# Kernel tuning notes

Measured on AMD Instinct MI355X. Metric: run time of the kernel, lower is better.

Reference implementation:

```python
import jax, jax.numpy as jnp
import numpy as np

BN_EPS = 1e-5
NEG_SLOPE = 0.2

def _avgpool2(x):
    B, C, H, W = x.shape
    return x.reshape(B, C, H // 2, 2, W // 2, 2).mean(axis=(3, 5))

def _conv1x1(x, w, b):
    # x: [B,C,H,W], w: [O,C], b: [O]
    return jnp.einsum('bchw,oc->bohw', x, w) + b[None, :, None, None]

def _bilinear_resize(x, out_h, out_w):
    # PyTorch F.interpolate(mode='bilinear', align_corners=False) semantics
    B, C, h, w = x.shape
    ys = jnp.maximum((jnp.arange(out_h, dtype=jnp.float32) + 0.5) * (h / out_h) - 0.5, 0.0)
    xs = jnp.maximum((jnp.arange(out_w, dtype=jnp.float32) + 0.5) * (w / out_w) - 0.5, 0.0)
    y0 = jnp.floor(ys).astype(jnp.int32); x0 = jnp.floor(xs).astype(jnp.int32)
    wy = (ys - y0.astype(jnp.float32)).astype(x.dtype)
    wx = (xs - x0.astype(jnp.float32)).astype(x.dtype)
    y1 = jnp.minimum(y0 + 1, h - 1); x1 = jnp.minimum(x0 + 1, w - 1)
    rows = x[:, :, y0, :] * (1.0 - wy)[None, None, :, None] + x[:, :, y1, :] * wy[None, None, :, None]
    out = rows[:, :, :, x0] * (1.0 - wx)[None, None, None, :] + rows[:, :, :, x1] * wx[None, None, None, :]
    return out

def setup_inputs() -> dict:
    key = jax.random.key(0)
    ks = jax.random.split(key, 16)
    B, Cin, Hid, Cout, H, W = 8, 64, 64, 64, 128, 128
    s = 0.05
    return {
        'rgb': jax.random.normal(ks[0], (B, Cin, H, W), dtype=jnp.float32),
        'freq': jax.random.normal(ks[1], (B, Cin, H, W), dtype=jnp.float32),
        'w_q': jax.random.normal(ks[2], (Hid, Cin), dtype=jnp.float32) * s,
        'b_q': jax.random.normal(ks[3], (Hid,), dtype=jnp.float32) * s,
        'w_k': jax.random.normal(ks[4], (Hid, Cin), dtype=jnp.float32) * s,
        'b_k': jax.random.normal(ks[5], (Hid,), dtype=jnp.float32) * s,
        'w_v': jax.random.normal(ks[6], (Hid, Cin), dtype=jnp.float32) * s,
        'b_v': jax.random.normal(ks[7], (Hid,), dtype=jnp.float32) * s,
        'w_o': jax.random.normal(ks[8], (Cout, Hid), dtype=jnp.float32) * s,
        'b_o': jax.random.normal(ks[9], (Cout,), dtype=jnp.float32) * s,
        'bn_gamma': jnp.ones((Cout,), dtype=jnp.float32),
        'bn_beta': jnp.zeros((Cout,), dtype=jnp.float32),
        'bn_mean': jax.random.normal(ks[10], (Cout,), dtype=jnp.float32) * s,
        'bn_var': jax.random.uniform(ks[11], (Cout,), dtype=jnp.float32, minval=0.5, maxval=1.5),
    }

def reference(rgb, freq, w_q, b_q, w_k, b_k, w_v, b_v, w_o, b_o, bn_gamma, bn_beta, bn_mean, bn_var):
    B, C, H, W = rgb.shape
    rgb_ds = _avgpool2(rgb)
    freq_ds = _avgpool2(freq)
    hd, wd = rgb_ds.shape[2], rgb_ds.shape[3]
    hid = w_q.shape[0]
    scale = hid ** (-0.5)
    # 1x1 conv QKV projections, flatten spatial dims to tokens N = hd*wd
    q = _conv1x1(rgb_ds, w_q, b_q).reshape(B, hid, hd * wd)   # [B,hid,N]
    k = _conv1x1(freq_ds, w_k, b_k).reshape(B, hid, hd * wd)  # [B,hid,N]
    v = _conv1x1(freq_ds, w_v, b_v).reshape(B, hid, hd * wd)  # [B,hid,N]
    attn = jax.nn.softmax(jnp.einsum('bcn,bcm->bnm', q, k) * scale, axis=-1)  # [B,N,N]
    z = jnp.einsum('bnm,bcm->bcn', attn, v).reshape(B, hid, hd, wd)
    z = _bilinear_resize(z, H, W)
    y = _conv1x1(z, w_o, b_o)
    # inference-mode BatchNorm fused as affine
    inv = bn_gamma / jnp.sqrt(bn_var + BN_EPS)
    y = (y - bn_mean[None, :, None, None]) * inv[None, :, None, None] + bn_beta[None, :, None, None]
    y = jnp.where(y >= 0, y, NEG_SLOPE * y)  # LeakyReLU(0.2)
    return rgb + y
```

## Files before the change

kernel.cpp:

```cpp
#include <hip/hip_runtime.h>
#include <hip/hip_bf16.h>

typedef unsigned short u16;
typedef unsigned int   u32;
typedef __attribute__((ext_vector_type(8))) short bf16x8;
typedef __attribute__((ext_vector_type(4))) float f32x4;

__device__ __forceinline__ u16 f2bf(float f) {
  u32 u = __float_as_uint(f);
  u32 r = u + 0x7fffu + ((u >> 16) & 1u);
  return (u16)(r >> 16);
}
__device__ __forceinline__ float bflo(u32 u) { return __uint_as_float(u << 16); }
__device__ __forceinline__ float bfhi(u32 u) { return __uint_as_float(u & 0xffff0000u); }
__device__ __forceinline__ u32 packhi(float a, float b) {
  return __builtin_amdgcn_perm(__float_as_uint(b), __float_as_uint(a), 0x07060302u);
}

__global__ __launch_bounds__(256, 4) void k_qkv(
    const float* __restrict__ rgb, const float* __restrict__ freq,
    const float* __restrict__ wq, const float* __restrict__ bq,
    const float* __restrict__ wk, const float* __restrict__ bk,
    const float* __restrict__ wv, const float* __restrict__ bv,
    u16* __restrict__ Qo, u16* __restrict__ Ko, u16* __restrict__ Vo)
{
  __shared__ __align__(16) u16 sm[3 * 4608];
  u16* X  = sm;
  u16* W0 = sm + 4608;
  u16* W1 = sm + 9216;

  const int t    = threadIdx.x;
  const int side = blockIdx.x & 1;
  const int seg  = blockIdx.x >> 1;
  const int idx0 = seg * 64;
  const int bb   = idx0 >> 12;
  const int n0   = idx0 & 4095;
  const int h    = n0 >> 6;
  const float* src = side ? freq : rgb;

  const size_t sbase = (size_t)bb * 64 * 16384 + (size_t)(2 * h) * 128;
  for (int i = 0; i < 2; ++i) {
    int cell = i * 256 + t;
    int tok  = cell & 63;
    int grp  = cell >> 6;
    const float* p0 = src + sbase + 2 * tok + (size_t)(grp * 8) * 16384;
    u32 pk[4];
#pragma unroll
    for (int cc = 0; cc < 8; cc += 2) {
      const float* pa = p0 + (size_t)cc * 16384;
      float2 a0 = *(const float2*)pa;
      float2 a1 = *(const float2*)(pa + 128);
      float v0 = 0.25f * ((a0.x + a0.y) + (a1.x + a1.y));
      const float* pb = pa + 16384;
      float2 b0 = *(const float2*)pb;
      float2 b1 = *(const float2*)(pb + 128);
      float v1 = 0.25f * ((b0.x + b0.y) + (b1.x + b1.y));
      pk[cc >> 1] = (u32)f2bf(v0) | ((u32)f2bf(v1) << 16);
    }
    uint4 q4; q4.x = pk[0]; q4.y = pk[1]; q4.z = pk[2]; q4.w = pk[3];
    *(uint4*)&X[tok * 72 + grp * 8] = q4;
  }
  {
    const int o = t >> 2, c0 = (t & 3) << 4;
    const float4* p4 = (const float4*)((side ? wk : wq) + o * 64 + c0);
    float4 f0 = p4[0], f1 = p4[1], f2 = p4[2], f3 = p4[3];
    uint4 qa, qb;
    qa.x = (u32)f2bf(f0.x) | ((u32)f2bf(f0.y) << 16);
    qa.y = (u32)f2bf(f0.z) | ((u32)f2bf(f0.w) << 16);
    qa.z = (u32)f2bf(f1.x) | ((u32)f2bf(f1.y) << 16);
    qa.w = (u32)f2bf(f1.z) | ((u32)f2bf(f1.w) << 16);
    qb.x = (u32)f2bf(f2.x) | ((u32)f2bf(f2.y) << 16);
    qb.y = (u32)f2bf(f2.z) | ((u32)f2bf(f2.w) << 16);
    qb.z = (u32)f2bf(f3.x) | ((u32)f2bf(f3.y) << 16);
    qb.w = (u32)f2bf(f3.z) | ((u32)f2bf(f3.w) << 16);
    *(uint4*)&W0[o * 72 + c0] = qa;
    *(uint4*)&W0[o * 72 + c0 + 8] = qb;
    if (side) {
      const float4* v4 = (const float4*)(wv + o * 64 + c0);
      float4 g0 = v4[0], g1 = v4[1], g2 = v4[2], g3 = v4[3];
      qa.x = (u32)f2bf(g0.x) | ((u32)f2bf(g0.y) << 16);
      qa.y = (u32)f2bf(g0.z) | ((u32)f2bf(g0.w) << 16);
      qa.z = (u32)f2bf(g1.x) | ((u32)f2bf(g1.y) << 16);
      qa.w = (u32)f2bf(g1.z) | ((u32)f2bf(g1.w) << 16);
      qb.x = (u32)f2bf(g2.x) | ((u32)f2bf(g2.y) << 16);
      qb.y = (u32)f2bf(g2.z) | ((u32)f2bf(g2.w) << 16);
      qb.z = (u32)f2bf(g3.x) | ((u32)f2bf(g3.y) << 16);
      qb.w = (u32)f2bf(g3.z) | ((u32)f2bf(g3.w) << 16);
      *(uint4*)&W1[o * 72 + c0] = qa;
      *(uint4*)&W1[o * 72 + c0 + 8] = qb;
    }
  }
  __syncthreads();

  const int lane = t & 63, w = t >> 6;
  const int l15 = lane & 15, qd = lane >> 4;
  const int tb = w * 16;

  bf16x8 af0 = *(const bf16x8*)&X[(tb + l15) * 72 + qd * 8];
  bf16x8 af1 = *(const bf16x8*)&X[(tb + l15) * 72 + 32 + qd * 8];

  f32x4 acc[4];
#pragma unroll
  for (int nt = 0; nt < 4; ++nt) {
    bf16x8 b0 = *(const bf16x8*)&W0[(nt * 16 + l15) * 72 + qd * 8];
    bf16x8 b1 = *(const bf16x8*)&W0[(nt * 16 + l15) * 72 + 32 + qd * 8];
    f32x4 a = {0.f, 0.f, 0.f, 0.f};
    a = __builtin_amdgcn_mfma_f32_16x16x32_bf16(af0, b0, a, 0, 0, 0);
    a = __builtin_amdgcn_mfma_f32_16x16x32_bf16(af1, b1, a, 0, 0, 0);
    acc[nt] = a;
  }
  {
    const float* bias0 = side ? bk : bq;
    const float sc = side ? 1.f : 0.125f;
    u16* dst0 = side ? Ko : Qo;
#pragma unroll
    for (int nt = 0; nt < 4; ++nt) {
      float bia = bias0[nt * 16 + l15];
#pragma unroll
      for (int e = 0; e < 4; ++e) {
        int tok = idx0 + tb + qd * 4 + e;
        dst0[(size_t)tok * 64 + nt * 16 + l15] = f2bf((acc[nt][e] + bia) * sc);
      }
    }
  }

  if (side) {
    f32x4 accv[4];
#pragma unroll
    for (int ct = 0; ct < 4; ++ct) {
      bf16x8 a0 = *(const bf16x8*)&W1[(ct * 16 + l15) * 72 + qd * 8];
      bf16x8 a1 = *(const bf16x8*)&W1[(ct * 16 + l15) * 72 + 32 + qd * 8];
      f32x4 a = {0.f, 0.f, 0.f, 0.f};
      a = __builtin_amdgcn_mfma_f32_16x16x32_bf16(a0, af0, a, 0, 0, 0);
      a = __builtin_amdgcn_mfma_f32_16x16x32_bf16(a1, af1, a, 0, 0, 0);
      accv[ct] = a;
    }
#pragma unroll
    for (int ct = 0; ct < 4; ++ct) {
#pragma unroll
      for (int e = 0; e < 4; ++e) {
        int c = ct * 16 + qd * 4 + e;
        float v = accv[ct][e] + bv[c];
        Vo[((size_t)(bb * 64 + c)) * 4096 + n0 + tb + l15] = f2bf(v);
      }
    }
  }
}

__global__ __launch_bounds__(256, 2) void k_attn(
    const u16* __restrict__ Qg, const u16* __restrict__ Kg,
    const u16* __restrict__ Vg,
    const float* __restrict__ wo, const float* __restrict__ bo,
    const float* __restrict__ gam, const float* __restrict__ bet,
    const float* __restrict__ mean, const float* __restrict__ var,
    u16* __restrict__ Ya)
{
  __shared__ __align__(16) u16 Pb[4 * 4608];
  __shared__ __align__(16) u16 Wl[4608];
  __shared__ __align__(16) u16 Zc[4608];
  __shared__ float lb[256];

  const int b  = blockIdx.x;
  const int q0 = blockIdx.y * 64;
  const int t  = threadIdx.x;
  const int lane = t & 63, w = t >> 6;
  const int l15 = lane & 15, qd = lane >> 4;
  u16* P = Pb + w * 4608;

  {
    const int o = t >> 2, c0 = (t & 3) << 4;
    const float4* p4 = (const float4*)(wo + o * 64 + c0);
    float4 f0 = p4[0], f1 = p4[1], f2 = p4[2], f3 = p4[3];
    uint4 qa, qb;
    qa.x = (u32)f2bf(f0.x) | ((u32)f2bf(f0.y) << 16);
    qa.y = (u32)f2bf(f0.z) | ((u32)f2bf(f0.w) << 16);
    qa.z = (u32)f2bf(f1.x) | ((u32)f2bf(f1.y) << 16);
    qa.w = (u32)f2bf(f1.z) | ((u32)f2bf(f1.w) << 16);
    qb.x = (u32)f2bf(f2.x) | ((u32)f2bf(f2.y) << 16);
    qb.y = (u32)f2bf(f2.z) | ((u32)f2bf(f2.w) << 16);
    qb.z = (u32)f2bf(f3.x) | ((u32)f2bf(f3.y) << 16);
    qb.w = (u32)f2bf(f3.z) | ((u32)f2bf(f3.w) << 16);
    *(uint4*)&Wl[o * 72 + c0] = qa;
    *(uint4*)&Wl[o * 72 + c0 + 8] = qb;
  }

  bf16x8 qf[4][2];
#pragma unroll
  for (int qt = 0; qt < 4; ++qt) {
    const u16* p = Qg + ((size_t)(b * 4096 + q0 + qt * 16 + l15)) * 64 + qd * 8;
    qf[qt][0] = *(const bf16x8*)p;
    qf[qt][1] = *(const bf16x8*)(p + 32);
  }

  f32x4 zacc[4][4];
#pragma unroll
  for (int i = 0; i < 4; ++i)
#pragma unroll
    for (int j = 0; j < 4; ++j) {
      f32x4 z = {0.f, 0.f, 0.f, 0.f};
      zacc[i][j] = z;
    }
  float lacc[4] = {0.f, 0.f, 0.f, 0.f};

  for (int tile = 0; tile < 16; ++tile) {
    const int n0 = w * 1024 + tile * 64;

    bf16x8 kf[4][2], vf[4][2];
#pragma unroll
    for (int mt = 0; mt < 4; ++mt) {
      const u16* p = Kg + ((size_t)(b * 4096 + n0 + mt * 16 + l15)) * 64 + qd * 8;
      kf[mt][0] = *(const bf16x8*)p;
      kf[mt][1] = *(const bf16x8*)(p + 32);
    }
#pragma unroll
    for (int ct = 0; ct < 4; ++ct) {
      const u16* p = Vg + ((size_t)(b * 64 + ct * 16 + l15)) * 4096 + n0 + qd * 8;
      vf[ct][0] = *(const bf16x8*)p;
      vf[ct][1] = *(const bf16x8*)(p + 32);
    }

#pragma unroll
    for (int qt = 0; qt < 4; ++qt) {
#pragma unroll
      for (int mt = 0; mt < 4; ++mt) {
        f32x4 a = {0.f, 0.f, 0.f, 0.f};
        a = __builtin_amdgcn_mfma_f32_16x16x32_bf16(kf[mt][0], qf[qt][0], a, 0, 0, 0);
        a = __builtin_amdgcn_mfma_f32_16x16x32_bf16(kf[mt][1], qf[qt][1], a, 0, 0, 0);
        float p0 = __expf(a[0]);
        float p1 = __expf(a[1]);
        float p2 = __expf(a[2]);
        float p3 = __expf(a[3]);
        lacc[qt] += (p0 + p1) + (p2 + p3);
        uint2 pw;
        pw.x = packhi(p0, p1);
        pw.y = packhi(p2, p3);
        *(uint2*)&P[(qt * 16 + l15) * 72 + mt * 16 + qd * 4] = pw;
      }
    }
#pragma unroll
    for (int qt = 0; qt < 4; ++qt) {
      bf16x8 pf0 = *(const bf16x8*)&P[(qt * 16 + l15) * 72 + qd * 8];
      bf16x8 pf1 = *(const bf16x8*)&P[(qt * 16 + l15) * 72 + 32 + qd * 8];
#pragma unroll
      for (int ct = 0; ct < 4; ++ct) {
        zacc[ct][qt] = __builtin_amdgcn_mfma_f32_16x16x32_bf16(vf[ct][0], pf0, zacc[ct][qt], 0, 0, 0);
        zacc[ct][qt] = __builtin_amdgcn_mfma_f32_16x16x32_bf16(vf[ct][1], pf1, zacc[ct][qt], 0, 0, 0);
      }
    }
  }

#pragma unroll
  for (int qt = 0; qt < 4; ++qt) {
    float l = lacc[qt];
    l += __shfl_xor(l, 16);
    l += __shfl_xor(l, 32);
    lb[w * 64 + qt * 16 + l15] = l;
  }
#pragma unroll
  for (int qt = 0; qt < 4; ++qt)
#pragma unroll
    for (int ct = 0; ct < 4; ++ct) {
      uint2 pw;
      pw.x = packhi(zacc[ct][qt][0], zacc[ct][qt][1]);
      pw.y = packhi(zacc[ct][qt][2], zacc[ct][qt][3]);
      *(uint2*)&P[(qt * 16 + l15) * 72 + ct * 16 + qd * 4] = pw;
    }
  __syncthreads();

  {
    const u32* Pu = (const u32*)Pb;
    u32* Zu = (u32*)Zc;
#pragma unroll
    for (int i = 0; i < 8; ++i) {
      int cell = i * 256 + t;
      int q = cell >> 5, cu = cell & 31;
      float s0 = 0.f, s1 = 0.f;
#pragma unroll
      for (int ww = 0; ww < 4; ++ww) {
        u32 v = Pu[ww * 2304 + q * 36 + cu];
        s0 += bflo(v);
        s1 += bfhi(v);
      }
      float inv = 1.f / (lb[q] + lb[64 + q] + lb[128 + q] + lb[192 + q]);
      Zu[q * 36 + cu] = packhi(s0 * inv, s1 * inv);
    }
  }
  __syncthreads();

  {
    bf16x8 af0 = *(const bf16x8*)&Zc[(w * 16 + l15) * 72 + qd * 8];
    bf16x8 af1 = *(const bf16x8*)&Zc[(w * 16 + l15) * 72 + 32 + qd * 8];
#pragma unroll
    for (int nt = 0; nt < 4; ++nt) {
      bf16x8 b0 = *(const bf16x8*)&Wl[(nt * 16 + l15) * 72 + qd * 8];
      bf16x8 b1 = *(const bf16x8*)&Wl[(nt * 16 + l15) * 72 + 32 + qd * 8];
      f32x4 y = {0.f, 0.f, 0.f, 0.f};
      y = __builtin_amdgcn_mfma_f32_16x16x32_bf16(af0, b0, y, 0, 0, 0);
      y = __builtin_amdgcn_mfma_f32_16x16x32_bf16(af1, b1, y, 0, 0, 0);
      const int o = nt * 16 + l15;
      float A = gam[o] * __frsqrt_rn(var[o] + 1e-5f);
      float B = (bo[o] - mean[o]) * A + bet[o];
#pragma unroll
      for (int e = 0; e < 4; ++e) {
        float v = y[e] * A + B;
        size_t tok = (size_t)(b * 4096 + q0 + w * 16 + qd * 4 + e);
        Ya[tok * 64 + o] = (u16)(__float_as_uint(v) >> 16);
      }
    }
  }
}

__global__ __launch_bounds__(256, 4) void k_out(
    const u16* __restrict__ Ya, const float* __restrict__ rgb,
    float* __restrict__ out)
{
  const int px = blockIdx.x * 256 + threadIdx.x;
  const int j = px & 127;
  const int i = (px >> 7) & 127;
  const int b = px >> 14;

  float ys = fmaxf((i + 0.5f) * 0.5f - 0.5f, 0.f);
  int   y0 = (int)ys;
  float wy = ys - (float)y0;
  int   y1 = min(y0 + 1, 63);
  float xs = fmaxf((j + 0.5f) * 0.5f - 0.5f, 0.f);
  int   x0 = (int)xs;
  float wx = xs - (float)x0;
  int   x1 = min(x0 + 1, 63);
  float w00 = (1.f - wy) * (1.f - wx), w01 = (1.f - wy) * wx;
  float w10 = wy * (1.f - wx),         w11 = wy * wx;

  const u16* yb = Ya + (size_t)b * 262144;
  const int b00 = (y0 * 64 + x0) * 64, b01 = (y0 * 64 + x1) * 64;
  const int b10 = (y1 * 64 + x0) * 64, b11 = (y1 * 64 + x1) * 64;

#pragma unroll
  for (int ch = 0; ch < 8; ++ch) {
    uint4 a00 = *(const uint4*)&yb[b00 + ch * 8];
    uint4 a01 = *(const uint4*)&yb[b01 + ch * 8];
    uint4 a10 = *(const uint4*)&yb[b10 + ch * 8];
    uint4 a11 = *(const uint4*)&yb[b11 + ch * 8];
    const u32* u00 = (const u32*)&a00;
    const u32* u01 = (const u32*)&a01;
    const u32* u10 = (const u32*)&a10;
    const u32* u11 = (const u32*)&a11;
#pragma unroll
    for (int e = 0; e < 8; ++e) {
      const int wd = e >> 1;
      float c00 = (e & 1) ? bfhi(u00[wd]) : bflo(u00[wd]);
      float c01 = (e & 1) ? bfhi(u01[wd]) : bflo(u01[wd]);
      float c10 = (e & 1) ? bfhi(u10[wd]) : bflo(u10[wd]);
      float c11 = (e & 1) ? bfhi(u11[wd]) : bflo(u11[wd]);
      float v = w00 * c00 + w01 * c01 + w10 * c10 + w11 * c11;
      v = (v >= 0.f) ? v : 0.2f * v;
      const int o = ch * 8 + e;
      const size_t oi = ((size_t)((b * 64 + o) * 128 + i)) * 128 + j;
      out[oi] = rgb[oi] + v;
    }
  }
}

extern "C" void kernel_launch(void* const* d_in, const int* in_sizes, int n_in,
                              void* d_out, int out_size, void* d_ws, size_t ws_size,
                              hipStream_t stream) {
  (void)in_sizes; (void)n_in; (void)out_size; (void)ws_size;
  const float* rgb  = (const float*)d_in[0];
  const float* freq = (const float*)d_in[1];
  const float* wq   = (const float*)d_in[2];
  const float* bq   = (const float*)d_in[3];
  const float* wk   = (const float*)d_in[4];
  const float* bk   = (const float*)d_in[5];
  const float* wv   = (const float*)d_in[6];
  const float* bv   = (const float*)d_in[7];
  const float* wo   = (const float*)d_in[8];
  const float* bo   = (const float*)d_in[9];
  const float* gam  = (const float*)d_in[10];
  const float* bet  = (const float*)d_in[11];
  const float* mean = (const float*)d_in[12];
  const float* var  = (const float*)d_in[13];

  char* ws = (char*)d_ws;
  u16* Qw = (u16*)(ws);
  u16* Kw = (u16*)(ws + 4194304);
  u16* Vw = (u16*)(ws + 8388608);
  u16* Yw = (u16*)(ws + 12582912);

  k_qkv<<<dim3(1024), dim3(256), 0, stream>>>(rgb, freq, wq, bq, wk, bk, wv, bv,
                                              Qw, Kw, Vw);
  k_attn<<<dim3(8, 64), dim3(256), 0, stream>>>(Qw, Kw, Vw, wo, bo, gam, bet,
                                                mean, var, Yw);
  k_out<<<dim3(512), dim3(256), 0, stream>>>(Yw, rgb, (float*)d_out);
}
```

Baseline: 228.5 us.

## Split attention keys over 8 waves, swizzle LDS, use exp2, widen output grid

The attention kernel now runs 512 threads, with 8 waves each covering 512 keys instead of 4 waves covering 1024. The P scratch buffer switches to an XOR-swizzled layout with no padding, and the final reduction reuses that buffer, so the separate Wl and Zc buffers are dropped. The output weights are loaded straight into registers, the Q scale folds in log2(e) so exp2f replaces __expf, and the output kernel splits channels into four quarter-blocks, giving four times as many blocks. The aim is more parallelism, lower latency per block and fewer LDS bank conflicts, at the cost of more shared memory per block and a wider cross-wave reduction.

```diff
diff --git a/kernel.cpp b/kernel.cpp
--- a/kernel.cpp
+++ b/kernel.cpp
@@ -15,6 +15,9 @@
 __device__ __forceinline__ float bfhi(u32 u) { return __uint_as_float(u & 0xffff0000u); }
 __device__ __forceinline__ u32 packhi(float a, float b) {
   return __builtin_amdgcn_perm(__float_as_uint(b), __float_as_uint(a), 0x07060302u);
+}
+__device__ __forceinline__ int pidx(int r, int wo) {
+  return (r * 32 + (wo ^ ((r & 7) << 2))) * 2;
 }
 
 __global__ __launch_bounds__(256, 4) void k_qkv(
@@ -111,7 +114,7 @@
   }
   {
     const float* bias0 = side ? bk : bq;
-    const float sc = side ? 1.f : 0.125f;
+    const float sc = side ? 1.f : 0.18033688f;
     u16* dst0 = side ? Ko : Qo;
 #pragma unroll
     for (int nt = 0; nt < 4; ++nt) {
@@ -147,7 +150,7 @@
   }
 }
 
-__global__ __launch_bounds__(256, 2) void k_attn(
+__global__ __launch_bounds__(512, 4) void k_attn(
     const u16* __restrict__ Qg, const u16* __restrict__ Kg,
     const u16* __restrict__ Vg,
     const float* __restrict__ wo, const float* __restrict__ bo,
@@ -155,33 +158,34 @@
     const float* __restrict__ mean, const float* __restrict__ var,
     u16* __restrict__ Ya)
 {
-  __shared__ __align__(16) u16 Pb[4 * 4608];
-  __shared__ __align__(16) u16 Wl[4608];
-  __shared__ __align__(16) u16 Zc[4608];
-  __shared__ float lb[256];
+  __shared__ __align__(16) u16 Pb[8 * 4096];
+  __shared__ float lb[8 * 64];
 
   const int b  = blockIdx.x;
   const int q0 = blockIdx.y * 64;
   const int t  = threadIdx.x;
   const int lane = t & 63, w = t >> 6;
   const int l15 = lane & 15, qd = lane >> 4;
-  u16* P = Pb + w * 4608;
-
+  u16* P = Pb + w * 4096;
+
+  bf16x8 wf0, wf1;
   {
-    const int o = t >> 2, c0 = (t & 3) << 4;
-    const float4* p4 = (const float4*)(wo + o * 64 + c0);
-    float4 f0 = p4[0], f1 = p4[1], f2 = p4[2], f3 = p4[3];
-    uint4 qa, qb;
-    qa.x = (u32)f2bf(f0.x) | ((u32)f2bf(f0.y) << 16);
-    qa.y = (u32)f2bf(f0.z) | ((u32)f2bf(f0.w) << 16);
-    qa.z = (u32)f2bf(f1.x) | ((u32)f2bf(f1.y) << 16);
-    qa.w = (u32)f2bf(f1.z) | ((u32)f2bf(f1.w) << 16);
-    qb.x = (u32)f2bf(f2.x) | ((u32)f2bf(f2.y) << 16);
-    qb.y = (u32)f2bf(f2.z) | ((u32)f2bf(f2.w) << 16);
-    qb.z = (u32)f2bf(f3.x) | ((u32)f2bf(f3.y) << 16);
-    qb.w = (u32)f2bf(f3.z) | ((u32)f2bf(f3.w) << 16);
-    *(uint4*)&Wl[o * 72 + c0] = qa;
-    *(uint4*)&Wl[o * 72 + c0 + 8] = qb;
+    const float* wop = wo + (((w & 3) * 16 + l15) * 64);
+    float4 a0 = *(const float4*)(wop + qd * 8);
+    float4 a1 = *(const float4*)(wop + qd * 8 + 4);
+    float4 c0 = *(const float4*)(wop + 32 + qd * 8);
+    float4 c1 = *(const float4*)(wop + 32 + qd * 8 + 4);
+    union { u32 u[4]; bf16x8 v; } cv;
+    cv.u[0] = (u32)f2bf(a0.x) | ((u32)f2bf(a0.y) << 16);
+    cv.u[1] = (u32)f2bf(a0.z) | ((u32)f2bf(a0.w) << 16);
+    cv.u[2] = (u32)f2bf(a1.x) | ((u32)f2bf(a1.y) << 16);
+    cv.u[3] = (u32)f2bf(a1.z) | ((u32)f2bf(a1.w) << 16);
+    wf0 = cv.v;
+    cv.u[0] = (u32)f2bf(c0.x) | ((u32)f2bf(c0.y) << 16);
+    cv.u[1] = (u32)f2bf(c0.z) | ((u32)f2bf(c0.w) << 16);
+    cv.u[2] = (u32)f2bf(c1.x) | ((u32)f2bf(c1.y) << 16);
+    cv.u[3] = (u32)f2bf(c1.z) | ((u32)f2bf(c1.w) << 16);
+    wf1 = cv.v;
   }
 
   bf16x8 qf[4][2];
@@ -202,10 +206,11 @@
     }
   float lacc[4] = {0.f, 0.f, 0.f, 0.f};
 
-  for (int tile = 0; tile < 16; ++tile) {
-    const int n0 = w * 1024 + tile * 64;
-
-    bf16x8 kf[4][2], vf[4][2];
+#pragma unroll 1
+  for (int tile = 0; tile < 8; ++tile) {
+    const int n0 = w * 512 + tile * 64;
+
+    bf16x8 kf[4][2];
 #pragma unroll
     for (int mt = 0; mt < 4; ++mt) {
       const u16* p = Kg + ((size_t)(b * 4096 + n0 + mt * 16 + l15)) * 64 + qd * 8;
@@ -213,34 +218,34 @@
       kf[mt][1] = *(const bf16x8*)(p + 32);
     }
 #pragma unroll
+    for (int qt = 0; qt < 4; ++qt) {
+#pragma unroll
+      for (int mt = 0; mt < 4; ++mt) {
+        f32x4 a = {0.f, 0.f, 0.f, 0.f};
+        a = __builtin_amdgcn_mfma_f32_16x16x32_bf16(kf[mt][0], qf[qt][0], a, 0, 0, 0);
+        a = __builtin_amdgcn_mfma_f32_16x16x32_bf16(kf[mt][1], qf[qt][1], a, 0, 0, 0);
+        float p0 = exp2f(a[0]);
+        float p1 = exp2f(a[1]);
+        float p2 = exp2f(a[2]);
+        float p3 = exp2f(a[3]);
+        lacc[qt] += (p0 + p1) + (p2 + p3);
+        uint2 pw;
+        pw.x = packhi(p0, p1);
+        pw.y = packhi(p2, p3);
+        *(uint2*)&P[pidx(qt * 16 + l15, mt * 8 + qd * 2)] = pw;
+      }
+    }
+    bf16x8 vf[4][2];
+#pragma unroll
     for (int ct = 0; ct < 4; ++ct) {
       const u16* p = Vg + ((size_t)(b * 64 + ct * 16 + l15)) * 4096 + n0 + qd * 8;
       vf[ct][0] = *(const bf16x8*)p;
       vf[ct][1] = *(const bf16x8*)(p + 32);
     }
-
 #pragma unroll
     for (int qt = 0; qt < 4; ++qt) {
-#pragma unroll
-      for (int mt = 0; mt < 4; ++mt) {
-        f32x4 a = {0.f, 0.f, 0.f, 0.f};
-        a = __builtin_amdgcn_mfma_f32_16x16x32_bf16(kf[mt][0], qf[qt][0], a, 0, 0, 0);
-        a = __builtin_amdgcn_mfma_f32_16x16x32_bf16(kf[mt][1], qf[qt][1], a, 0, 0, 0);
-        float p0 = __expf(a[0]);
-        float p1 = __expf(a[1]);
-        float p2 = __expf(a[2]);
-        float p3 = __expf(a[3]);
-        lacc[qt] += (p0 + p1) + (p2 + p3);
-        uint2 pw;
-        pw.x = packhi(p0, p1);
-        pw.y = packhi(p2, p3);
-        *(uint2*)&P[(qt * 16 + l15) * 72 + mt * 16 + qd * 4] = pw;
-      }
-    }
-#pragma unroll
-    for (int qt = 0; qt < 4; ++qt) {
-      bf16x8 pf0 = *(const bf16x8*)&P[(qt * 16 + l15) * 72 + qd * 8];
-      bf16x8 pf1 = *(const bf16x8*)&P[(qt * 16 + l15) * 72 + 32 + qd * 8];
+      bf16x8 pf0 = *(const bf16x8*)&P[pidx(qt * 16 + l15, qd * 4)];
+      bf16x8 pf1 = *(const bf16x8*)&P[pidx(qt * 16 + l15, 16 + qd * 4)];
 #pragma unroll
       for (int ct = 0; ct < 4; ++ct) {
         zacc[ct][qt] = __builtin_amdgcn_mfma_f32_16x16x32_bf16(vf[ct][0], pf0, zacc[ct][qt], 0, 0, 0);
@@ -254,7 +259,7 @@
     float l = lacc[qt];
     l += __shfl_xor(l, 16);
     l += __shfl_xor(l, 32);
-    lb[w * 64 + qt * 16 + l15] = l;
+    if (qd == 0) lb[w * 64 + qt * 16 + l15] = l;
   }
 #pragma unroll
   for (int qt = 0; qt < 4; ++qt)
@@ -263,58 +268,63 @@
       uint2 pw;
       pw.x = packhi(zacc[ct][qt][0], zacc[ct][qt][1]);
       pw.y = packhi(zacc[ct][qt][2], zacc[ct][qt][3]);
-      *(uint2*)&P[(qt * 16 + l15) * 72 + ct * 16 + qd * 4] = pw;
+      *(uint2*)&P[pidx(qt * 16 + l15, ct * 8 + qd * 2)] = pw;
     }
   __syncthreads();
 
   {
-    const u32* Pu = (const u32*)Pb;
-    u32* Zu = (u32*)Zc;
-#pragma unroll
-    for (int i = 0; i < 8; ++i) {
-      int cell = i * 256 + t;
+    const u32* Pw = (const u32*)Pb;
+    u32* Zw = (u32*)Pb;
+#pragma unroll
+    for (int i = 0; i < 4; ++i) {
+      int cell = i * 512 + t;
       int q = cell >> 5, cu = cell & 31;
-      float s0 = 0.f, s1 = 0.f;
-#pragma unroll
-      for (int ww = 0; ww < 4; ++ww) {
-        u32 v = Pu[ww * 2304 + q * 36 + cu];
+      int off = q * 32 + (cu ^ ((q & 7) << 2));
+      float s0 = 0.f, s1 = 0.f, ds = 0.f;
+#pragma unroll
+      for (int ww = 0; ww < 8; ++ww) {
+        u32 v = Pw[ww * 2048 + off];
         s0 += bflo(v);
         s1 += bfhi(v);
-      }
-      float inv = 1.f / (lb[q] + lb[64 + q] + lb[128 + q] + lb[192 + q]);
-      Zu[q * 36 + cu] = packhi(s0 * inv, s1 * inv);
+        ds += lb[ww * 64 + q];
+      }
+      float inv = 1.f / ds;
+      Zw[(q >> 4) * 2048 + off] = packhi(s0 * inv, s1 * inv);
     }
   }
   __syncthreads();
 
   {
-    bf16x8 af0 = *(const bf16x8*)&Zc[(w * 16 + l15) * 72 + qd * 8];
-    bf16x8 af1 = *(const bf16x8*)&Zc[(w * 16 + l15) * 72 + 32 + qd * 8];
-#pragma unroll
-    for (int nt = 0; nt < 4; ++nt) {
-      bf16x8 b0 = *(const bf16x8*)&Wl[(nt * 16 + l15) * 72 + qd * 8];
-      bf16x8 b1 = *(const bf16x8*)&Wl[(nt * 16 + l15) * 72 + 32 + qd * 8];
+    const int nt = w & 3;
+#pragma unroll
+    for (int k = 0; k < 2; ++k) {
+      const int qt = (w >> 2) * 2 + k;
+      const int r = qt * 16 + l15;
+      const u16* Zr = Pb + qt * 4096;
+      bf16x8 af0 = *(const bf16x8*)&Zr[pidx(r, qd * 4)];
+      bf16x8 af1 = *(const bf16x8*)&Zr[pidx(r, 16 + qd * 4)];
       f32x4 y = {0.f, 0.f, 0.f, 0.f};
-      y = __builtin_amdgcn_mfma_f32_16x16x32_bf16(af0, b0, y, 0, 0, 0);
-      y = __builtin_amdgcn_mfma_f32_16x16x32_bf16(af1, b1, y, 0, 0, 0);
+      y = __builtin_amdgcn_mfma_f32_16x16x32_bf16(af0, wf0, y, 0, 0, 0);
+      y = __builtin_amdgcn_mfma_f32_16x16x32_bf16(af1, wf1, y, 0, 0, 0);
       const int o = nt * 16 + l15;
       float A = gam[o] * __frsqrt_rn(var[o] + 1e-5f);
       float B = (bo[o] - mean[o]) * A + bet[o];
 #pragma unroll
       for (int e = 0; e < 4; ++e) {
         float v = y[e] * A + B;
-        size_t tok = (size_t)(b * 4096 + q0 + w * 16 + qd * 4 + e);
+        size_t tok = (size_t)(b * 4096 + q0 + qt * 16 + qd * 4 + e);
         Ya[tok * 64 + o] = (u16)(__float_as_uint(v) >> 16);
       }
     }
   }
 }
 
-__global__ __launch_bounds__(256, 4) void k_out(
+__global__ __launch_bounds__(256, 8) void k_out(
     const u16* __restrict__ Ya, const float* __restrict__ rgb,
     float* __restrict__ out)
 {
-  const int px = blockIdx.x * 256 + threadIdx.x;
+  const int cq = blockIdx.x >> 9;
+  const int px = (blockIdx.x & 511) * 256 + threadIdx.x;
   const int j = px & 127;
   const int i = (px >> 7) & 127;
   const int b = px >> 14;
@@ -330,12 +340,12 @@
   float w00 = (1.f - wy) * (1.f - wx), w01 = (1.f - wy) * wx;
   float w10 = wy * (1.f - wx),         w11 = wy * wx;
 
-  const u16* yb = Ya + (size_t)b * 262144;
+  const u16* yb = Ya + (size_t)b * 262144 + cq * 16;
   const int b00 = (y0 * 64 + x0) * 64, b01 = (y0 * 64 + x1) * 64;
   const int b10 = (y1 * 64 + x0) * 64, b11 = (y1 * 64 + x1) * 64;
 
 #pragma unroll
-  for (int ch = 0; ch < 8; ++ch) {
+  for (int ch = 0; ch < 2; ++ch) {
     uint4 a00 = *(const uint4*)&yb[b00 + ch * 8];
     uint4 a01 = *(const uint4*)&yb[b01 + ch * 8];
     uint4 a10 = *(const uint4*)&yb[b10 + ch * 8];
@@ -353,7 +363,7 @@
       float c11 = (e & 1) ? bfhi(u11[wd]) : bflo(u11[wd]);
       float v = w00 * c00 + w01 * c01 + w10 * c10 + w11 * c11;
       v = (v >= 0.f) ? v : 0.2f * v;
-      const int o = ch * 8 + e;
+      const int o = cq * 16 + ch * 8 + e;
       const size_t oi = ((size_t)((b * 64 + o) * 128 + i)) * 128 + j;
       out[oi] = rgb[oi] + v;
     }
@@ -387,7 +397,7 @@
 
   k_qkv<<<dim3(1024), dim3(256), 0, stream>>>(rgb, freq, wq, bq, wk, bk, wv, bv,
                                               Qw, Kw, Vw);
-  k_attn<<<dim3(8, 64), dim3(256), 0, stream>>>(Qw, Kw, Vw, wo, bo, gam, bet,
+  k_attn<<<dim3(8, 64), dim3(512), 0, stream>>>(Qw, Kw, Vw, wo, bo, gam, bet,
                                                 mean, var, Yw);
-  k_out<<<dim3(512), dim3(256), 0, stream>>>(Yw, rgb, (float*)d_out);
-}
+  k_out<<<dim3(2048), dim3(256), 0, stream>>>(Yw, rgb, (float*)d_out);
+}
```

Result: slower. 313.9 us (+37.4%).
